# Kernel tuning notes

Measured on AMD Instinct MI355X. Metric: run time of the kernel, lower is better.

Reference implementation:

```python
import jax, jax.numpy as jnp
import numpy as np

N = 50000      # nodes
E = 400000     # edges (before self-loops)
IN = 128       # input feature dim
HID = 32       # out_channels per head
HEADS = 12
NC = 2         # num_classes
SLOPE = 0.2    # GATv2 leaky_relu negative slope


def setup_inputs() -> dict:
    key = jax.random.key(0)
    ks = jax.random.split(key, 24)
    f32 = jnp.float32
    def nrm(k, shape, s=0.1):
        return jax.random.normal(k, shape, dtype=f32) * s
    inp = {}
    inp["x"] = jax.random.normal(ks[0], (N, IN), dtype=f32)
    inp["edge_index"] = jax.random.randint(ks[1], (2, E), 0, N, dtype=jnp.int32)
    # GATv2 layer 0: in=IN, layer 1: in=HID; both heads=HEADS, out=HID, concat=False
    dims = [IN, HID]
    i = 2
    for l, d in enumerate(dims):
        inp[f"Wl{l}"] = nrm(ks[i], (d, HEADS * HID)); i += 1
        inp[f"bl{l}"] = jnp.zeros((HEADS * HID,), f32)
        inp[f"Wr{l}"] = nrm(ks[i], (d, HEADS * HID)); i += 1
        inp[f"br{l}"] = jnp.zeros((HEADS * HID,), f32)
        inp[f"att{l}"] = nrm(ks[i], (HEADS, HID)); i += 1
        inp[f"bias{l}"] = jnp.zeros((HID,), f32)
    # output GATv2Conv(HID, NC): heads=1, concat=True
    inp["Wlo"] = nrm(ks[i], (HID, NC)); i += 1
    inp["blo"] = jnp.zeros((NC,), f32)
    inp["Wro"] = nrm(ks[i], (HID, NC)); i += 1
    inp["bro"] = jnp.zeros((NC,), f32)
    inp["atto"] = nrm(ks[i], (1, NC)); i += 1
    inp["biaso"] = jnp.zeros((NC,), f32)
    return inp


def gatv2_conv(x, src, dst, Wl, bl, Wr, br, att, bias, heads, out_ch, concat):
    """PyG GATv2Conv (share_weights=False, self-loops pre-appended, eval mode)."""
    n = x.shape[0]
    xl = (x @ Wl + bl).reshape(n, heads, out_ch)   # source transform
    xr = (x @ Wr + br).reshape(n, heads, out_ch)   # target transform
    # per-edge attention: e_ij = att . leaky_relu(xl_j + xr_i)
    h = jax.nn.leaky_relu(xl[src] + xr[dst], SLOPE)            # [E, H, C]
    logits = jnp.einsum('ehc,hc->eh', h, att)                   # [E, H]
    # segment softmax over incoming edges per destination node
    m = jax.ops.segment_max(logits, dst, num_segments=n)        # [N, H]
    a = jnp.exp(logits - m[dst])
    denom = jax.ops.segment_sum(a, dst, num_segments=n)         # [N, H]
    alpha = a / (denom[dst] + 1e-16)                            # [E, H]
    out = jax.ops.segment_sum(xl[src] * alpha[..., None], dst, num_segments=n)
    out = out.reshape(n, heads * out_ch) if concat else out.mean(axis=1)
    return out + bias


def reference(x, edge_index, Wl0, bl0, Wr0, br0, att0, bias0,
              Wl1, bl1, Wr1, br1, att1, bias1,
              Wlo, blo, Wro, bro, atto, biaso):
    n = x.shape[0]
    loop = jnp.arange(n, dtype=edge_index.dtype)
    src = jnp.concatenate([edge_index[0], loop])  # add self-loops (PyG default)
    dst = jnp.concatenate([edge_index[1], loop])
    h = gatv2_conv(x, src, dst, Wl0, bl0, Wr0, br0, att0, bias0, HEADS, HID, False)
    h = jax.nn.elu(h)
    h = gatv2_conv(h, src, dst, Wl1, bl1, Wr1, br1, att1, bias1, HEADS, HID, False)
    h = jax.nn.elu(h)
    out = gatv2_conv(h, src, dst, Wlo, blo, Wro, bro, atto, biaso, 1, NC, True)
    return out
```

## Files before the change

### kernel.cpp

```cpp
#include <hip/hip_runtime.h>
#include <hip/hip_fp16.h>
#include <math.h>

#define IN_DIM 128
#define HID 32
#define HEADS 12
#define FDIM (HEADS*HID)
#define SLOPE 0.2f
#define LOG2E 1.44269504f

typedef __attribute__((ext_vector_type(8))) short short8;
typedef __attribute__((ext_vector_type(4))) float float4v;
typedef __attribute__((ext_vector_type(4))) float f32x4;
typedef _Float16 hv2 __attribute__((ext_vector_type(2)));

__device__ __forceinline__ float dot2acc(hv2 a, hv2 b, float c) {
#if __has_builtin(__builtin_amdgcn_fdot2)
    return __builtin_amdgcn_fdot2(a, b, c, false);
#else
    return c + (float)a.x * (float)b.x + (float)a.y * (float)b.y;
#endif
}

__device__ __forceinline__ float exp2h(float x) {
#if __has_builtin(__builtin_amdgcn_exp2f)
    return __builtin_amdgcn_exp2f(x);
#else
    return exp2f(x);
#endif
}

__device__ __forceinline__ float fma_mix_lo(hv2 x, float a, float c) {
    float d;
    asm("v_fma_mix_f32 %0, %1, %2, %3 op_sel_hi:[1,0,0]"
        : "=v"(d) : "v"(x), "v"(a), "v"(c));
    return d;
}
__device__ __forceinline__ float fma_mix_hi(hv2 x, float a, float c) {
    float d;
    asm("v_fma_mix_f32 %0, %1, %2, %3 op_sel:[1,0,0] op_sel_hi:[1,0,0]"
        : "=v"(d) : "v"(x), "v"(a), "v"(c));
    return d;
}

__device__ __forceinline__ void async_cp16(const void* g, void* l) {
    __builtin_amdgcn_global_load_lds(
        (const __attribute__((address_space(1))) void*)g,
        (__attribute__((address_space(3))) void*)l, 16, 0, 0);
}


__global__ void hist_kernel(const int* __restrict__ dst, int* __restrict__ cnt, int E) {
    int e = blockIdx.x * blockDim.x + threadIdx.x;
    if (e < E) atomicAdd(&cnt[dst[e]], 1);
}

__global__ __launch_bounds__(256) void scan_partial_kernel(const int* __restrict__ cnt,
                                                           int* __restrict__ partials, int n) {
    int i = blockIdx.x * 256 + threadIdx.x;
    int v = (i < n) ? cnt[i] + 1 : 0;
#pragma unroll
    for (int off = 1; off < 64; off <<= 1) v += __shfl_xor(v, off);
    __shared__ int sh[4];
    if ((threadIdx.x & 63) == 0) sh[threadIdx.x >> 6] = v;
    __syncthreads();
    if (threadIdx.x == 0) partials[blockIdx.x] = sh[0] + sh[1] + sh[2] + sh[3];
}

__global__ __launch_bounds__(1024) void scan_top_kernel(int* __restrict__ partials, int nb) {
    __shared__ int sh[1024];
    int t = threadIdx.x;
    int v = (t < nb) ? partials[t] : 0;
    sh[t] = v;
    __syncthreads();
    for (int off = 1; off < 1024; off <<= 1) {
        int u = (t >= off) ? sh[t - off] : 0;
        __syncthreads();
        sh[t] += u;
        __syncthreads();
    }
    if (t < nb) partials[t] = sh[t] - v;
}

__global__ __launch_bounds__(256) void scan_final_kernel(const int* __restrict__ cnt,
                                                         const int* __restrict__ partials,
                                                         int* __restrict__ start,
                                                         int* __restrict__ cursor,
                                                         int* __restrict__ srcs,
                                                         int* __restrict__ srcsOff, int n) {
    __shared__ int sh[256];
    int t = threadIdx.x;
    int i = blockIdx.x * 256 + t;
    int v = (i < n) ? cnt[i] + 1 : 0;
    sh[t] = v;
    __syncthreads();
    for (int off = 1; off < 256; off <<= 1) {
        int u = (t >= off) ? sh[t - off] : 0;
        __syncthreads();
        sh[t] += u;
        __syncthreads();
    }
    int ex = sh[t] - v + partials[blockIdx.x];
    if (i < n) {
        start[i] = ex;
        cursor[i] = ex;
        int slot = ex + v - 1;
        srcs[slot] = i;
        srcsOff[slot] = i * (FDIM * 2);
        if (i == n - 1) start[n] = ex + v;
    }
}

__global__ void scatter_kernel(const int* __restrict__ src, const int* __restrict__ dst,
                               int* __restrict__ cursor, int* __restrict__ srcs,
                               int* __restrict__ srcsOff, int E) {
    int e = blockIdx.x * blockDim.x + threadIdx.x;
    if (e < E) {
        int d = dst[e];
        int pos = atomicAdd(&cursor[d], 1);
        int s = src[e];
        srcs[pos] = s;
        srcsOff[pos] = s * (FDIM * 2);
    }
}


__device__ __forceinline__ unsigned int bf16_rne(float f) {
    unsigned int u = __float_as_uint(f);
    return (u + 0x7FFFu + ((u >> 16) & 1u)) >> 16;
}


__global__ void prep_conv(const float* __restrict__ x, short* __restrict__ Ah,
                          short* __restrict__ Al, int total4, int convBlocks,
                          const float* __restrict__ Wl0, const float* __restrict__ Wr0,
                          const float* __restrict__ Wl1, const float* __restrict__ Wr1,
                          const float* __restrict__ a0, const float* __restrict__ a1,
                          short* __restrict__ Bl0h, short* __restrict__ Bl0l,
                          short* __restrict__ Br0h, short* __restrict__ Br0l,
                          short* __restrict__ Bl1h, short* __restrict__ Bl1l,
                          short* __restrict__ Br1h, short* __restrict__ Br1l,
                          _Float16* __restrict__ attH) {
    if (blockIdx.x < (unsigned)convBlocks) {
        int i = blockIdx.x * 256 + threadIdx.x;
        if (i >= total4) return;
        float4 v = ((const float4*)x)[i];
        float fs[4] = {v.x, v.y, v.z, v.w};
        unsigned int hb[4], lb[4];
#pragma unroll
        for (int t = 0; t < 4; t++) {
            hb[t] = bf16_rne(fs[t]);
            lb[t] = bf16_rne(fs[t] - __uint_as_float(hb[t] << 16));
        }
        uint2 hp, lp;
        hp.x = hb[0] | (hb[1] << 16); hp.y = hb[2] | (hb[3] << 16);
        lp.x = lb[0] | (lb[1] << 16); lp.y = lb[2] | (lb[3] << 16);
        ((uint2*)Ah)[i] = hp;
        ((uint2*)Al)[i] = lp;
        return;
    }
    int idx = (blockIdx.x - convBlocks) * 256 + threadIdx.x;
    if (idx < 49152) {
        int k = idx / 384, n = idx - k * 384;
        float w1 = Wl0[idx], w2 = Wr0[idx];
        unsigned int h1 = bf16_rne(w1);
        unsigned int l1 = bf16_rne(w1 - __uint_as_float(h1 << 16));
        unsigned int h2 = bf16_rne(w2);
        unsigned int l2 = bf16_rne(w2 - __uint_as_float(h2 << 16));
        Bl0h[n * 128 + k] = (short)h1;  Bl0l[n * 128 + k] = (short)l1;
        Br0h[n * 128 + k] = (short)h2;  Br0l[n * 128 + k] = (short)l2;
    } else if (idx < 61440) {
        int i2 = idx - 49152;
        int k = i2 / 384, n = i2 - k * 384;
        float w1 = Wl1[i2], w2 = Wr1[i2];
        unsigned int h1 = bf16_rne(w1);
        unsigned int l1 = bf16_rne(w1 - __uint_as_float(h1 << 16));
        unsigned int h2 = bf16_rne(w2);
        unsigned int l2 = bf16_rne(w2 - __uint_as_float(h2 << 16));
        Bl1h[n * 32 + k] = (short)h1;  Bl1l[n * 32 + k] = (short)l1;
        Br1h[n * 32 + k] = (short)h2;  Br1l[n * 32 + k] = (short)l2;
    } else if (idx < 62208) {
        int i2 = idx - 61440;
        attH[i2] = (_Float16)(((i2 < 384) ? a0[i2] : a1[i2 - 384]) * LOG2E);
    }
}


__global__ __launch_bounds__(256) void gemm_pair_async(
    const short* __restrict__ Ahi, const short* __restrict__ Alo,
    const short* __restrict__ B1h, const short* __restrict__ B1l,
    const float* __restrict__ bias1, __half* __restrict__ C1,
    const short* __restrict__ B2h, const short* __restrict__ B2l,
    const float* __restrict__ bias2, __half* __restrict__ C2,
    int M, int K) {
    __shared__ __align__(16) unsigned char smem[33792];
    int tid = threadIdx.x;
    int lane = tid & 63;
    int wave = tid >> 6;
    int wm = wave & 1, wn = wave >> 1;
    int rowBase = blockIdx.x * 128;
    bool second = blockIdx.y >= 3;
    int colBase = (blockIdx.y - (second ? 3 : 0)) * 128;
    const short* Bh  = second ? B2h : B1h;
    const short* Bl  = second ? B2l : B1l;
    const float* bias = second ? bias2 : bias1;
    __half*      C    = second ? C2 : C1;

    const short8* AsHi = (const short8*)smem;
    const short8* AsLo = (const short8*)(smem + 8192);
    const short8* BsHi = (const short8*)(smem + 16384);
    const short8* BsLo = (const short8*)(smem + 24576);

    const short* gsrc[8];
    void* ldst[8];
#pragma unroll
    for (int q = 0; q < 8; q++) {
        int t  = (q & 1) * 4 + wave;
        int rc = t * 16 + (lane & 15);
        int ko = (lane >> 4) * 8;
        const short* base = (q < 2) ? Ahi : (q < 4) ? Alo : (q < 6) ? Bh : Bl;
        int rb = (q < 4) ? rowBase : colBase;
        gsrc[q] = base + (long)(rb + rc) * K + ko;
        ldst[q] = (void*)(smem + q * 4096 + wave * 1024);
    }

    float4v acc[4][4];
#pragma unroll
    for (int i = 0; i < 4; i++)
#pragma unroll
        for (int j = 0; j < 4; j++) acc[i][j] = (float4v){0.f, 0.f, 0.f, 0.f};

    for (int kt = 0; kt < K; kt += 32) {
#pragma unroll
        for (int q = 0; q < 8; q++) {
            async_cp16(gsrc[q], ldst[q]);
            gsrc[q] += 32;
        }
        __syncthreads();

        short8 ah[4], al[4], bh[4], blv[4];
#pragma unroll
        for (int i = 0; i < 4; i++) {
            ah[i]  = AsHi[(wm * 4 + i) * 64 + lane];
            al[i]  = AsLo[(wm * 4 + i) * 64 + lane];
            bh[i]  = BsHi[(wn * 4 + i) * 64 + lane];
            blv[i] = BsLo[(wn * 4 + i) * 64 + lane];
        }
#pragma unroll
        for (int i = 0; i < 4; i++)
#pragma unroll
            for (int j = 0; j < 4; j++) {
                acc[i][j] = __builtin_amdgcn_mfma_f32_16x16x32_bf16(ah[i], bh[j],  acc[i][j], 0, 0, 0);
                acc[i][j] = __builtin_amdgcn_mfma_f32_16x16x32_bf16(ah[i], blv[j], acc[i][j], 0, 0, 0);
                acc[i][j] = __builtin_amdgcn_mfma_f32_16x16x32_bf16(al[i], bh[j],  acc[i][j], 0, 0, 0);
            }
        __syncthreads();
    }

    float* Ct = (float*)smem;
    int cq = lane >> 4, cn = lane & 15;
#pragma unroll
    for (int ph = 0; ph < 2; ph++) {
        if (wm == ph) {
#pragma unroll
            for (int i = 0; i < 4; i++)
#pragma unroll
                for (int j = 0; j < 4; j++) {
                    int lr = i * 16 + cq * 4;
                    int lc = wn * 64 + j * 16 + cn;
#pragma unroll
                    for (int r = 0; r < 4; r++)
                        Ct[(lr + r) * 132 + lc] = acc[i][j][r];
                }
        }
        __syncthreads();
#pragma unroll
        for (int k = 0; k < 4; k++) {
            int o = k * 256 + tid;
            int lr = o >> 4;
            int oc = (o & 15) << 3;
            int gr = rowBase + ph * 64 + lr;
            if (gr < M) {
                float4 f0 = *(float4*)&Ct[lr * 132 + oc];
                float4 f1 = *(float4*)&Ct[lr * 132 + oc + 4];
                int gc = colBase + oc;
                float4 b0 = *(const float4*)(bias + gc);
                float4 b1 = *(const float4*)(bias + gc + 4);
                __half2 p0 = __floats2half2_rn(f0.x + b0.x, f0.y + b0.y);
                __half2 p1 = __floats2half2_rn(f0.z + b0.z, f0.w + b0.w);
                __half2 p2 = __floats2half2_rn(f1.x + b1.x, f1.y + b1.y);
                __half2 p3 = __floats2half2_rn(f1.z + b1.z, f1.w + b1.w);
                uint4 ov;
                ov.x = *(unsigned int*)&p0;
                ov.y = *(unsigned int*)&p1;
                ov.z = *(unsigned int*)&p2;
                ov.w = *(unsigned int*)&p3;
                *(uint4*)(C + (size_t)gr * FDIM + gc) = ov;
            }
        }
        __syncthreads();
    }
}


__global__ __launch_bounds__(64) void agg_kernel(const __half* __restrict__ xl,
                                                 const __half* __restrict__ xr,
                                                 const _Float16* __restrict__ att_h,
                                                 const float* __restrict__ bias,
                                                 const int* __restrict__ start,
                                                 const int* __restrict__ srcsOff,
                                                 short* __restrict__ houtHi,
                                                 short* __restrict__ houtLo,
                                                 const float* __restrict__ Wl,
                                                 const float* __restrict__ bl,
                                                 const float* __restrict__ Wr,
                                                 const float* __restrict__ br,
                                                 float* __restrict__ xloB,
                                                 float* __restrict__ xroB, int N) {
    int node = blockIdx.x;
    if (node >= N) return;
    int lane = threadIdx.x & 63;
    int hl = lane & 31;
    int half_ = lane >> 5;
    int cb = hl << 3;

    long nodeOff = (long)node * (FDIM * 2);
    hv2 xr2[6], at2[6];
    f32x4 acc[3];
    float s[3];
#pragma unroll
    for (int c = 0; c < 3; c++) {
        uint2 ur = *(const uint2*)((const char*)xr + nodeOff + c * 256 + cb);
        xr2[2*c]   = __builtin_bit_cast(hv2, ur.x);
        xr2[2*c+1] = __builtin_bit_cast(hv2, ur.y);
        uint2 ua = *(const uint2*)((const char*)att_h + c * 256 + cb);
        at2[2*c]   = __builtin_bit_cast(hv2, ua.x);
        at2[2*c+1] = __builtin_bit_cast(hv2, ua.y);
        acc[c] = (f32x4){0.f, 0.f, 0.f, 0.f};
        s[c] = 0.f;
    }
    const hv2 sl2 = {(_Float16)SLOPE, (_Float16)SLOPE};
    const char* xlb = (const char*)xl + cb;

    int e0 = start[node], e1 = start[node + 1];
    int b = e0;

    for (; b + 4 <= e1; b += 4) {
        hv2 xa[2][6];
#pragma unroll
        for (int p = 0; p < 2; p++) {
            const char* base = xlb + (long)srcsOff[b + p * 2 + half_];
            uint2 u0 = *(const uint2*)(base);
            uint2 u1 = *(const uint2*)(base + 256);
            uint2 u2 = *(const uint2*)(base + 512);
            xa[p][0] = __builtin_bit_cast(hv2, u0.x); xa[p][1] = __builtin_bit_cast(hv2, u0.y);
            xa[p][2] = __builtin_bit_cast(hv2, u1.x); xa[p][3] = __builtin_bit_cast(hv2, u1.y);
            xa[p][4] = __builtin_bit_cast(hv2, u2.x); xa[p][5] = __builtin_bit_cast(hv2, u2.y);
        }
#pragma unroll
        for (int p = 0; p < 2; p++) {
            float pc[3];
#pragma unroll
            for (int c = 0; c < 3; c++) {
                hv2 t0 = xa[p][2*c]   + xr2[2*c];
                hv2 t1 = xa[p][2*c+1] + xr2[2*c+1];
                t0 = __builtin_elementwise_max(t0, t0 * sl2);
                t1 = __builtin_elementwise_max(t1, t1 * sl2);
                pc[c] = dot2acc(t1, at2[2*c+1], dot2acc(t0, at2[2*c], 0.f));
            }
#pragma unroll
            for (int st = 1; st <= 4; st <<= 1) {
                pc[0] += __shfl_xor(pc[0], st);
                pc[1] += __shfl_xor(pc[1], st);
                pc[2] += __shfl_xor(pc[2], st);
            }
#pragma unroll
            for (int c = 0; c < 3; c++) {
                float a = exp2h(pc[c]);
                s[c] += a;
                acc[c].x = fma_mix_lo(xa[p][2*c],   a, acc[c].x);
                acc[c].y = fma_mix_hi(xa[p][2*c],   a, acc[c].y);
                acc[c].z = fma_mix_lo(xa[p][2*c+1], a, acc[c].z);
                acc[c].w = fma_mix_hi(xa[p][2*c+1], a, acc[c].w);
            }
        }
    }

    if (b < e1) {
        hv2 xa[2][6];
        float mask[2];
#pragma unroll
        for (int p = 0; p < 2; p++) {
            int myIdx = b + p * 2 + half_;
            int ic = min(myIdx, e1 - 1);
            mask[p] = (myIdx < e1) ? 0.f : -1e30f;
            const char* base = xlb + (long)srcsOff[ic];
            uint2 u0 = *(const uint2*)(base);
            uint2 u1 = *(const uint2*)(base + 256);
            uint2 u2 = *(const uint2*)(base + 512);
            xa[p][0] = __builtin_bit_cast(hv2, u0.x); xa[p][1] = __builtin_bit_cast(hv2, u0.y);
            xa[p][2] = __builtin_bit_cast(hv2, u1.x); xa[p][3] = __builtin_bit_cast(hv2, u1.y);
            xa[p][4] = __builtin_bit_cast(hv2, u2.x); xa[p][5] = __builtin_bit_cast(hv2, u2.y);
        }
#pragma unroll
        for (int p = 0; p < 2; p++) {
            float pc[3];
#pragma unroll
            for (int c = 0; c < 3; c++) {
                hv2 t0 = xa[p][2*c]   + xr2[2*c];
                hv2 t1 = xa[p][2*c+1] + xr2[2*c+1];
                t0 = __builtin_elementwise_max(t0, t0 * sl2);
                t1 = __builtin_elementwise_max(t1, t1 * sl2);
                pc[c] = dot2acc(t1, at2[2*c+1], dot2acc(t0, at2[2*c], 0.f));
            }
#pragma unroll
            for (int st = 1; st <= 4; st <<= 1) {
                pc[0] += __shfl_xor(pc[0], st);
                pc[1] += __shfl_xor(pc[1], st);
                pc[2] += __shfl_xor(pc[2], st);
            }
#pragma unroll
            for (int c = 0; c < 3; c++) {
                float a = exp2h(pc[c] + mask[p]);
                s[c] += a;
                acc[c].x = fma_mix_lo(xa[p][2*c],   a, acc[c].x);
                acc[c].y = fma_mix_hi(xa[p][2*c],   a, acc[c].y);
                acc[c].z = fma_mix_lo(xa[p][2*c+1], a, acc[c].z);
                acc[c].w = fma_mix_hi(xa[p][2*c+1], a, acc[c].w);
            }
        }
    }

#pragma unroll
    for (int c = 0; c < 3; c++) {
        acc[c].x += __shfl_xor(acc[c].x, 32);
        acc[c].y += __shfl_xor(acc[c].y, 32);
        acc[c].z += __shfl_xor(acc[c].z, 32);
        acc[c].w += __shfl_xor(acc[c].w, 32);
        s[c] += __shfl_xor(s[c], 32);
    }
    f32x4 v[3];
#pragma unroll
    for (int c = 0; c < 3; c++) {
        float inv = 1.f / (s[c] + 1e-16f);
        f32x4 iv = {inv, inv, inv, inv};
        v[c] = acc[c] * iv;
    }
#pragma unroll
    for (int st = 8; st <= 16; st <<= 1) {
#pragma unroll
        for (int c = 0; c < 3; c++) {
            v[c].x += __shfl_xor(v[c].x, st);
            v[c].y += __shfl_xor(v[c].y, st);
            v[c].z += __shfl_xor(v[c].z, st);
            v[c].w += __shfl_xor(v[c].w, st);
        }
    }
    if (lane < 8) {
        f32x4 b4 = *(const f32x4*)(bias + (hl << 2));
        f32x4 o = (v[0] + v[1] + v[2]) * (f32x4){1.f/12.f, 1.f/12.f, 1.f/12.f, 1.f/12.f} + b4;
        o.x = o.x > 0.f ? o.x : expm1f(o.x);
        o.y = o.y > 0.f ? o.y : expm1f(o.y);
        o.z = o.z > 0.f ? o.z : expm1f(o.z);
        o.w = o.w > 0.f ? o.w : expm1f(o.w);
        if (houtHi) {
            float fs[4] = {o.x, o.y, o.z, o.w};
            unsigned int hb[4], lb[4];
#pragma unroll
            for (int t = 0; t < 4; t++) {
                hb[t] = bf16_rne(fs[t]);
                lb[t] = bf16_rne(fs[t] - __uint_as_float(hb[t] << 16));
            }
            uint2 hp, lp;
            hp.x = hb[0] | (hb[1] << 16); hp.y = hb[2] | (hb[3] << 16);
            lp.x = lb[0] | (lb[1] << 16); lp.y = lb[2] | (lb[3] << 16);
            *(uint2*)(houtHi + (size_t)node * 32 + (hl << 2)) = hp;
            *(uint2*)(houtLo + (size_t)node * 32 + (hl << 2)) = lp;
        }
        if (Wl) {
            f32x4 wl0 = *(const f32x4*)(Wl + (hl << 3));
            f32x4 wl1 = *(const f32x4*)(Wl + (hl << 3) + 4);
            f32x4 wr0 = *(const f32x4*)(Wr + (hl << 3));
            f32x4 wr1 = *(const f32x4*)(Wr + (hl << 3) + 4);
            float l0 = o.x * wl0.x + o.y * wl0.z + o.z * wl1.x + o.w * wl1.z;
            float l1 = o.x * wl0.y + o.y * wl0.w + o.z * wl1.y + o.w * wl1.w;
            float r0 = o.x * wr0.x + o.y * wr0.z + o.z * wr1.x + o.w * wr1.z;
            float r1 = o.x * wr0.y + o.y * wr0.w + o.z * wr1.y + o.w * wr1.w;
#pragma unroll
            for (int st = 1; st <= 4; st <<= 1) {
                l0 += __shfl_xor(l0, st); l1 += __shfl_xor(l1, st);
                r0 += __shfl_xor(r0, st); r1 += __shfl_xor(r1, st);
            }
            if (hl == 0) {
                xloB[2 * node]     = l0 + bl[0];
                xloB[2 * node + 1] = l1 + bl[1];
                xroB[2 * node]     = r0 + br[0];
                xroB[2 * node + 1] = r1 + br[1];
            }
        }
    }
}


__global__ __launch_bounds__(256) void out_agg_kernel(const float* __restrict__ xlo,
                                                      const float* __restrict__ xro,
                                                      const float* __restrict__ atto,
                                                      const float* __restrict__ biaso,
                                                      const int* __restrict__ start,
                                                      const int* __restrict__ srcs,
                                                      float* __restrict__ out, int N) {
    int g = (blockIdx.x * blockDim.x + threadIdx.x) >> 3;
    int j = threadIdx.x & 7;
    if (g >= N) return;
    float a0 = atto[0] * LOG2E, a1 = atto[1] * LOG2E;
    float xr0 = xro[2 * g], xr1 = xro[2 * g + 1];
    float s = 0.f, acc0 = 0.f, acc1 = 0.f;
    int e0 = start[g], e1 = start[g + 1];
    for (int idx = e0 + j; idx < e1; idx += 8) {
        int jj = srcs[idx];
        float x0 = xlo[2 * jj], x1 = xlo[2 * jj + 1];
        float t0 = x0 + xr0, t1 = x1 + xr1;
        t0 = fmaxf(t0, SLOPE * t0);
        t1 = fmaxf(t1, SLOPE * t1);
        float a = exp2h(a0 * t0 + a1 * t1);
        s += a;
        acc0 = fmaf(a, x0, acc0);
        acc1 = fmaf(a, x1, acc1);
    }
#pragma unroll
    for (int st = 1; st <= 4; st <<= 1) {
        s    += __shfl_xor(s, st);
        acc0 += __shfl_xor(acc0, st);
        acc1 += __shfl_xor(acc1, st);
    }
    if (j == 0) {
        float inv = 1.0f / (s + 1e-16f);
        out[2 * g]     = acc0 * inv + biaso[0];
        out[2 * g + 1] = acc1 * inv + biaso[1];
    }
}


extern "C" void kernel_launch(void* const* d_in, const int* in_sizes, int n_in,
                              void* d_out, int out_size, void* d_ws, size_t ws_size,
                              hipStream_t stream) {
    const float* x    = (const float*)d_in[0];
    const int*   ei   = (const int*)d_in[1];
    const float* Wl0  = (const float*)d_in[2];
    const float* bl0  = (const float*)d_in[3];
    const float* Wr0  = (const float*)d_in[4];
    const float* br0  = (const float*)d_in[5];
    const float* att0 = (const float*)d_in[6];
    const float* bias0= (const float*)d_in[7];
    const float* Wl1  = (const float*)d_in[8];
    const float* bl1  = (const float*)d_in[9];
    const float* Wr1  = (const float*)d_in[10];
    const float* br1  = (const float*)d_in[11];
    const float* att1 = (const float*)d_in[12];
    const float* bias1= (const float*)d_in[13];
    const float* Wlo  = (const float*)d_in[14];
    const float* blo  = (const float*)d_in[15];
    const float* Wro  = (const float*)d_in[16];
    const float* bro  = (const float*)d_in[17];
    const float* atto = (const float*)d_in[18];
    const float* biaso= (const float*)d_in[19];

    const int N = in_sizes[0] / IN_DIM;
    const int E = in_sizes[1] / 2;

    char* ws = (char*)d_ws;
    size_t off = 0;
    auto take = [&](size_t bytes) -> char* {
        char* p = ws + off;
        off += (bytes + 255) & ~(size_t)255;
        return p;
    };
    __half* xlf = (__half*)take((size_t)N * FDIM * 2);
    __half* xrf = (__half*)take((size_t)N * FDIM * 2);
    float* xloB = (float*)take((size_t)N * 2 * 4);
    float* xroB = (float*)take((size_t)N * 2 * 4);
    int* cnt    = (int*)take((size_t)N * 4);
    int* startA = (int*)take((size_t)(N + 1) * 4);
    int* cursor = (int*)take((size_t)N * 4);
    int* srcs   = (int*)take((size_t)(E + N) * 4);
    int* srcsOff= (int*)take((size_t)(E + N) * 4);
    int  nb     = (N + 255) / 256;
    int* partials = (int*)take((size_t)nb * 4);
    short* Bl0h = (short*)take((size_t)FDIM * IN_DIM * 2);
    short* Bl0l = (short*)take((size_t)FDIM * IN_DIM * 2);
    short* Br0h = (short*)take((size_t)FDIM * IN_DIM * 2);
    short* Br0l = (short*)take((size_t)FDIM * IN_DIM * 2);
    short* Bl1h = (short*)take((size_t)FDIM * HID * 2);
    short* Bl1l = (short*)take((size_t)FDIM * HID * 2);
    short* Br1h = (short*)take((size_t)FDIM * HID * 2);
    short* Br1l = (short*)take((size_t)FDIM * HID * 2);
    short* xh   = (short*)take((size_t)N * IN_DIM * 2);
    short* xlo_ = (short*)take((size_t)N * IN_DIM * 2);
    short* h0h  = (short*)take((size_t)N * HID * 2);
    short* h0l  = (short*)take((size_t)N * HID * 2);
    _Float16* attH = (_Float16*)take((size_t)768 * 2);
    (void)take(32768);

    const int* esrc = ei;
    const int* edst = ei + E;

    int total4 = N * IN_DIM / 4;
    int convBlocks = (total4 + 255) / 256;
    prep_conv<<<convBlocks + 243, 256, 0, stream>>>(x, xh, xlo_, total4, convBlocks,
                                                    Wl0, Wr0, Wl1, Wr1, att0, att1,
                                                    Bl0h, Bl0l, Br0h, Br0l,
                                                    Bl1h, Bl1l, Br1h, Br1l, attH);

    hipMemsetAsync(cnt, 0, (size_t)N * 4, stream);
    hist_kernel<<<(E + 255) / 256, 256, 0, stream>>>(edst, cnt, E);
    scan_partial_kernel<<<nb, 256, 0, stream>>>(cnt, partials, N);
    scan_top_kernel<<<1, 1024, 0, stream>>>(partials, nb);
    scan_final_kernel<<<nb, 256, 0, stream>>>(cnt, partials, startA, cursor, srcs, srcsOff, N);
    scatter_kernel<<<(E + 255) / 256, 256, 0, stream>>>(esrc, edst, cursor, srcs, srcsOff, E);

    dim3 ggrid((N + 127) / 128, 6);
    gemm_pair_async<<<ggrid, 256, 0, stream>>>(xh, xlo_, Bl0h, Bl0l, bl0, xlf, Br0h, Br0l, br0, xrf, N, IN_DIM);
    agg_kernel<<<N, 64, 0, stream>>>(xlf, xrf, attH, bias0, startA, srcsOff,
                                     h0h, h0l, nullptr, nullptr, nullptr, nullptr,
                                     nullptr, nullptr, N);
    gemm_pair_async<<<ggrid, 256, 0, stream>>>(h0h, h0l, Bl1h, Bl1l, bl1, xlf, Br1h, Br1l, br1, xrf, N, HID);
    agg_kernel<<<N, 64, 0, stream>>>(xlf, xrf, attH + 384, bias1, startA, srcsOff,
                                     nullptr, nullptr, Wlo, blo, Wro, bro,
                                     xloB, xroB, N);
    out_agg_kernel<<<((size_t)N * 8 + 255) / 256, 256, 0, stream>>>(xloB, xroB, atto, biaso, startA, srcs, (float*)d_out, N);
}
```

Measured before the change: 374.6 us.

## Fuse histogram into prep kernel, drop scan_top kernel, prefetch edge offsets

```diff
diff --git a/kernel.cpp b/kernel.cpp
--- a/kernel.cpp
+++ b/kernel.cpp
@@ -50,11 +50,6 @@
 }
 
 
-__global__ void hist_kernel(const int* __restrict__ dst, int* __restrict__ cnt, int E) {
-    int e = blockIdx.x * blockDim.x + threadIdx.x;
-    if (e < E) atomicAdd(&cnt[dst[e]], 1);
-}
-
 __global__ __launch_bounds__(256) void scan_partial_kernel(const int* __restrict__ cnt,
                                                            int* __restrict__ partials, int n) {
     int i = blockIdx.x * 256 + threadIdx.x;
@@ -65,21 +60,6 @@
     if ((threadIdx.x & 63) == 0) sh[threadIdx.x >> 6] = v;
     __syncthreads();
     if (threadIdx.x == 0) partials[blockIdx.x] = sh[0] + sh[1] + sh[2] + sh[3];
-}
-
-__global__ __launch_bounds__(1024) void scan_top_kernel(int* __restrict__ partials, int nb) {
-    __shared__ int sh[1024];
-    int t = threadIdx.x;
-    int v = (t < nb) ? partials[t] : 0;
-    sh[t] = v;
-    __syncthreads();
-    for (int off = 1; off < 1024; off <<= 1) {
-        int u = (t >= off) ? sh[t - off] : 0;
-        __syncthreads();
-        sh[t] += u;
-        __syncthreads();
-    }
-    if (t < nb) partials[t] = sh[t] - v;
 }
 
 __global__ __launch_bounds__(256) void scan_final_kernel(const int* __restrict__ cnt,
@@ -89,18 +69,26 @@
                                                          int* __restrict__ srcs,
                                                          int* __restrict__ srcsOff, int n) {
     __shared__ int sh[256];
+    __shared__ int ps[4];
     int t = threadIdx.x;
+    int pv = 0;
+    for (int j = t; j < blockIdx.x; j += 256) pv += partials[j];
+#pragma unroll
+    for (int off = 1; off < 64; off <<= 1) pv += __shfl_xor(pv, off);
+    if ((t & 63) == 0) ps[t >> 6] = pv;
+
     int i = blockIdx.x * 256 + t;
     int v = (i < n) ? cnt[i] + 1 : 0;
     sh[t] = v;
     __syncthreads();
+    int base = ps[0] + ps[1] + ps[2] + ps[3];
     for (int off = 1; off < 256; off <<= 1) {
         int u = (t >= off) ? sh[t - off] : 0;
         __syncthreads();
         sh[t] += u;
         __syncthreads();
     }
-    int ex = sh[t] - v + partials[blockIdx.x];
+    int ex = sh[t] - v + base;
     if (i < n) {
         start[i] = ex;
         cursor[i] = ex;
@@ -140,7 +128,8 @@
                           short* __restrict__ Br0h, short* __restrict__ Br0l,
                           short* __restrict__ Bl1h, short* __restrict__ Bl1l,
                           short* __restrict__ Br1h, short* __restrict__ Br1l,
-                          _Float16* __restrict__ attH) {
+                          _Float16* __restrict__ attH,
+                          const int* __restrict__ edst, int* __restrict__ cnt, int E) {
     if (blockIdx.x < (unsigned)convBlocks) {
         int i = blockIdx.x * 256 + threadIdx.x;
         if (i >= total4) return;
@@ -159,30 +148,35 @@
         ((uint2*)Al)[i] = lp;
         return;
     }
-    int idx = (blockIdx.x - convBlocks) * 256 + threadIdx.x;
-    if (idx < 49152) {
-        int k = idx / 384, n = idx - k * 384;
-        float w1 = Wl0[idx], w2 = Wr0[idx];
-        unsigned int h1 = bf16_rne(w1);
-        unsigned int l1 = bf16_rne(w1 - __uint_as_float(h1 << 16));
-        unsigned int h2 = bf16_rne(w2);
-        unsigned int l2 = bf16_rne(w2 - __uint_as_float(h2 << 16));
-        Bl0h[n * 128 + k] = (short)h1;  Bl0l[n * 128 + k] = (short)l1;
-        Br0h[n * 128 + k] = (short)h2;  Br0l[n * 128 + k] = (short)l2;
-    } else if (idx < 61440) {
-        int i2 = idx - 49152;
-        int k = i2 / 384, n = i2 - k * 384;
-        float w1 = Wl1[i2], w2 = Wr1[i2];
-        unsigned int h1 = bf16_rne(w1);
-        unsigned int l1 = bf16_rne(w1 - __uint_as_float(h1 << 16));
-        unsigned int h2 = bf16_rne(w2);
-        unsigned int l2 = bf16_rne(w2 - __uint_as_float(h2 << 16));
-        Bl1h[n * 32 + k] = (short)h1;  Bl1l[n * 32 + k] = (short)l1;
-        Br1h[n * 32 + k] = (short)h2;  Br1l[n * 32 + k] = (short)l2;
-    } else if (idx < 62208) {
-        int i2 = idx - 61440;
-        attH[i2] = (_Float16)(((i2 < 384) ? a0[i2] : a1[i2 - 384]) * LOG2E);
-    }
+    if (blockIdx.x < (unsigned)(convBlocks + 243)) {
+        int idx = (blockIdx.x - convBlocks) * 256 + threadIdx.x;
+        if (idx < 49152) {
+            int k = idx / 384, n = idx - k * 384;
+            float w1 = Wl0[idx], w2 = Wr0[idx];
+            unsigned int h1 = bf16_rne(w1);
+            unsigned int l1 = bf16_rne(w1 - __uint_as_float(h1 << 16));
+            unsigned int h2 = bf16_rne(w2);
+            unsigned int l2 = bf16_rne(w2 - __uint_as_float(h2 << 16));
+            Bl0h[n * 128 + k] = (short)h1;  Bl0l[n * 128 + k] = (short)l1;
+            Br0h[n * 128 + k] = (short)h2;  Br0l[n * 128 + k] = (short)l2;
+        } else if (idx < 61440) {
+            int i2 = idx - 49152;
+            int k = i2 / 384, n = i2 - k * 384;
+            float w1 = Wl1[i2], w2 = Wr1[i2];
+            unsigned int h1 = bf16_rne(w1);
+            unsigned int l1 = bf16_rne(w1 - __uint_as_float(h1 << 16));
+            unsigned int h2 = bf16_rne(w2);
+            unsigned int l2 = bf16_rne(w2 - __uint_as_float(h2 << 16));
+            Bl1h[n * 32 + k] = (short)h1;  Bl1l[n * 32 + k] = (short)l1;
+            Br1h[n * 32 + k] = (short)h2;  Br1l[n * 32 + k] = (short)l2;
+        } else if (idx < 62208) {
+            int i2 = idx - 61440;
+            attH[i2] = (_Float16)(((i2 < 384) ? a0[i2] : a1[i2 - 384]) * LOG2E);
+        }
+        return;
+    }
+    int e = (blockIdx.x - convBlocks - 243) * 256 + threadIdx.x;
+    if (e < E) atomicAdd(&cnt[edst[e]], 1);
 }
 
 
@@ -345,17 +339,30 @@
     int e0 = start[node], e1 = start[node + 1];
     int b = e0;
 
+    int offA0 = 0, offA1 = 0;
+    if (b + 4 <= e1) {
+        offA0 = srcsOff[b + half_];
+        offA1 = srcsOff[b + 2 + half_];
+    }
     for (; b + 4 <= e1; b += 4) {
+        int offN0 = srcsOff[b + 4 + half_];
+        int offN1 = srcsOff[b + 6 + half_];
         hv2 xa[2][6];
-#pragma unroll
-        for (int p = 0; p < 2; p++) {
-            const char* base = xlb + (long)srcsOff[b + p * 2 + half_];
-            uint2 u0 = *(const uint2*)(base);
-            uint2 u1 = *(const uint2*)(base + 256);
-            uint2 u2 = *(const uint2*)(base + 512);
-            xa[p][0] = __builtin_bit_cast(hv2, u0.x); xa[p][1] = __builtin_bit_cast(hv2, u0.y);
-            xa[p][2] = __builtin_bit_cast(hv2, u1.x); xa[p][3] = __builtin_bit_cast(hv2, u1.y);
-            xa[p][4] = __builtin_bit_cast(hv2, u2.x); xa[p][5] = __builtin_bit_cast(hv2, u2.y);
+        {
+            const char* base0 = xlb + (long)offA0;
+            uint2 u0 = *(const uint2*)(base0);
+            uint2 u1 = *(const uint2*)(base0 + 256);
+            uint2 u2 = *(const uint2*)(base0 + 512);
+            xa[0][0] = __builtin_bit_cast(hv2, u0.x); xa[0][1] = __builtin_bit_cast(hv2, u0.y);
+            xa[0][2] = __builtin_bit_cast(hv2, u1.x); xa[0][3] = __builtin_bit_cast(hv2, u1.y);
+            xa[0][4] = __builtin_bit_cast(hv2, u2.x); xa[0][5] = __builtin_bit_cast(hv2, u2.y);
+            const char* base1 = xlb + (long)offA1;
+            uint2 v0 = *(const uint2*)(base1);
+            uint2 v1 = *(const uint2*)(base1 + 256);
+            uint2 v2 = *(const uint2*)(base1 + 512);
+            xa[1][0] = __builtin_bit_cast(hv2, v0.x); xa[1][1] = __builtin_bit_cast(hv2, v0.y);
+            xa[1][2] = __builtin_bit_cast(hv2, v1.x); xa[1][3] = __builtin_bit_cast(hv2, v1.y);
+            xa[1][4] = __builtin_bit_cast(hv2, v2.x); xa[1][5] = __builtin_bit_cast(hv2, v2.y);
         }
 #pragma unroll
         for (int p = 0; p < 2; p++) {
@@ -384,6 +391,8 @@
                 acc[c].w = fma_mix_hi(xa[p][2*c+1], a, acc[c].w);
             }
         }
+        offA0 = offN0;
+        offA1 = offN1;
     }
 
     if (b < e1) {
@@ -604,17 +613,19 @@
     const int* esrc = ei;
     const int* edst = ei + E;
 
+    hipMemsetAsync(cnt, 0, (size_t)N * 4, stream);
+
     int total4 = N * IN_DIM / 4;
     int convBlocks = (total4 + 255) / 256;
-    prep_conv<<<convBlocks + 243, 256, 0, stream>>>(x, xh, xlo_, total4, convBlocks,
-                                                    Wl0, Wr0, Wl1, Wr1, att0, att1,
-                                                    Bl0h, Bl0l, Br0h, Br0l,
-                                                    Bl1h, Bl1l, Br1h, Br1l, attH);
-
-    hipMemsetAsync(cnt, 0, (size_t)N * 4, stream);
-    hist_kernel<<<(E + 255) / 256, 256, 0, stream>>>(edst, cnt, E);
+    int histBlocks = (E + 255) / 256;
+    prep_conv<<<convBlocks + 243 + histBlocks, 256, 0, stream>>>(
+        x, xh, xlo_, total4, convBlocks,
+        Wl0, Wr0, Wl1, Wr1, att0, att1,
+        Bl0h, Bl0l, Br0h, Br0l,
+        Bl1h, Bl1l, Br1h, Br1l, attH,
+        edst, cnt, E);
+
     scan_partial_kernel<<<nb, 256, 0, stream>>>(cnt, partials, N);
-    scan_top_kernel<<<1, 1024, 0, stream>>>(partials, nb);
     scan_final_kernel<<<nb, 256, 0, stream>>>(cnt, partials, startA, cursor, srcs, srcsOff, N);
     scatter_kernel<<<(E + 255) / 256, 256, 0, stream>>>(esrc, edst, cursor, srcs, srcsOff, E);
 
```

After: 367.0 us. 2.0% less time.
